# Performance work log

Measured on AMD Instinct MI355X. Metric: run time of the kernel, lower is better.

## Reference

```python
import jax, jax.numpy as jnp
import numpy as np

B, N, C = 16, 1024, 384
HEADS = 4
HIDDEN = 4 * C  # mlp_ratio=4 -> 1536
EPS = 1e-5


def layernorm(x, g, b):
    mu = jnp.mean(x, axis=-1, keepdims=True)
    var = jnp.mean((x - mu) ** 2, axis=-1, keepdims=True)
    return (x - mu) / jnp.sqrt(var + EPS) * g + b


def hardswish(x):
    return x * jnp.clip(x + 3.0, 0.0, 6.0) / 6.0


def setup_inputs() -> dict:
    key = jax.random.key(0)
    ks = jax.random.split(key, 8)
    s = 0.02
    return {
        "x": jax.random.normal(ks[0], (B, N, C), jnp.float32),
        "ln1_g": jnp.ones((C,), jnp.float32),
        "ln1_b": jnp.zeros((C,), jnp.float32),
        "Wqkv": jax.random.normal(ks[1], (3 * C, C), jnp.float32) * s,
        "Wproj": jax.random.normal(ks[2], (C, C), jnp.float32) * s,
        "bproj": jnp.zeros((C,), jnp.float32),
        "ln2_g": jnp.ones((C,), jnp.float32),
        "ln2_b": jnp.zeros((C,), jnp.float32),
        "Wfc1": jax.random.normal(ks[3], (HIDDEN, C, 1, 1), jnp.float32) * s,
        "bfc1": jnp.zeros((HIDDEN,), jnp.float32),
        "Wdw": jax.random.normal(ks[4], (HIDDEN, 1, 3, 3), jnp.float32) * s,
        "bdw": jnp.zeros((HIDDEN,), jnp.float32),
        "Wfc2": jax.random.normal(ks[5], (C, HIDDEN, 1, 1), jnp.float32) * s,
        "bfc2": jnp.zeros((C,), jnp.float32),
        "H": 32,
        "W": 32,
    }


def reference(x, ln1_g, ln1_b, Wqkv, Wproj, bproj, ln2_g, ln2_b,
              Wfc1, bfc1, Wdw, bdw, Wfc2, bfc2, H, W):
    b, n, c = x.shape
    h = HEADS
    hd = c // h
    # --- attention branch ---
    xn = layernorm(x, ln1_g, ln1_b)
    qkv = xn @ Wqkv.T  # [B,N,3C]
    qkv = qkv.reshape(b, n, h, 3, hd).transpose(3, 0, 2, 1, 4)  # [3,B,h,N,hd]
    q, k, v = qkv[0], qkv[1], qkv[2]
    attn = jax.nn.softmax(jnp.einsum('bhnd,bhmd->bhnm', q, k) * (hd ** -0.5), axis=-1)
    o = jnp.einsum('bhnm,bhmd->bhnd', attn, v)  # [B,h,N,hd]
    o = o.transpose(0, 2, 1, 3).reshape(b, n, c)
    o = o @ Wproj.T + bproj
    x = x + o
    # --- IRB (inverted residual conv MLP) branch ---
    y = layernorm(x, ln2_g, ln2_b)
    y = y.transpose(0, 2, 1).reshape(b, c, H, W)  # NCHW
    dn = ('NCHW', 'OIHW', 'NCHW')
    y = jax.lax.conv_general_dilated(y, Wfc1, (1, 1), 'VALID', dimension_numbers=dn)
    y = hardswish(y + bfc1[None, :, None, None])
    y = jax.lax.conv_general_dilated(y, Wdw, (1, 1), 'SAME',
                                     feature_group_count=Wdw.shape[0],
                                     dimension_numbers=dn)
    y = hardswish(y + bdw[None, :, None, None])
    y = jax.lax.conv_general_dilated(y, Wfc2, (1, 1), 'VALID', dimension_numbers=dn)
    y = y + bfc2[None, :, None, None]
    y = y.reshape(b, c, n).transpose(0, 2, 1)
    return x + y
```

## Files before the change

kernel.cpp:

```cpp
#include <hip/hip_runtime.h>
#include <hip/hip_bf16.h>
#include <math.h>

#define BB 16
#define NN 1024
#define CC 384
#define HEADS 4
#define HD 96
#define HID 1536
#define MROWS (BB*NN)

typedef __attribute__((ext_vector_type(8))) short bf16x8;
typedef __attribute__((ext_vector_type(4))) float f32x4;

__device__ __forceinline__ float hswish(float x) {
    float t = fminf(fmaxf(x + 3.0f, 0.0f), 6.0f);
    return x * t * (1.0f / 6.0f);
}

__device__ __forceinline__ ushort f2bf(float f) {
    union { float f; unsigned u; } v; v.f = f;
    unsigned r = v.u + 0x7fff + ((v.u >> 16) & 1);
    return (ushort)(r >> 16);
}

__device__ __forceinline__ float bf2f(ushort u) {
    union { unsigned u; float f; } v; v.u = ((unsigned)u) << 16;
    return v.f;
}

__device__ __forceinline__ void gload16(const ushort* g, ushort* l) {
    __builtin_amdgcn_global_load_lds(
        (const __attribute__((address_space(1))) void*)g,
        (__attribute__((address_space(3))) void*)l, 16, 0, 0);
}

#define S_QKV (1152*384)
#define S_P   (384*384)
#define S_1   (1536*384)
#define S_2   (384*1536)
__global__ __launch_bounds__(256) void wconv_all(
    const float* __restrict__ wqkv, const float* __restrict__ wproj,
    const float* __restrict__ wfc1, const float* __restrict__ wfc2,
    ushort* __restrict__ dq, ushort* __restrict__ dp,
    ushort* __restrict__ d1, ushort* __restrict__ d2)
{
    int i = blockIdx.x * 256 + threadIdx.x;
    if (i < S_QKV) {
        int row = i / 384;
        float v = wqkv[i];
        if ((row % 288) < 96) v *= 0.10206207261596577f;
        dq[i] = f2bf(v);
        return;
    }
    i -= S_QKV;
    if (i < S_P) { dp[i] = f2bf(wproj[i]); return; }
    i -= S_P;
    if (i < S_1) { d1[i] = f2bf(wfc1[i]); return; }
    i -= S_1;
    if (i < S_2) d2[i] = f2bf(wfc2[i]);
}

__global__ __launch_bounds__(256) void ln_kernel(
    const float* __restrict__ x, const float* __restrict__ g,
    const float* __restrict__ b, ushort* __restrict__ y)
{
    int row = blockIdx.x * 4 + (threadIdx.x >> 6);
    int lane = threadIdx.x & 63;
    const float* xr = x + (size_t)row * CC;
    float v[6];
    float s = 0.f;
#pragma unroll
    for (int j = 0; j < 6; ++j) { v[j] = xr[lane + 64 * j]; s += v[j]; }
#pragma unroll
    for (int off = 32; off; off >>= 1) s += __shfl_xor(s, off, 64);
    float mu = s * (1.0f / CC);
    float s2 = 0.f;
#pragma unroll
    for (int j = 0; j < 6; ++j) { float d = v[j] - mu; s2 += d * d; }
#pragma unroll
    for (int off = 32; off; off >>= 1) s2 += __shfl_xor(s2, off, 64);
    float rinv = rsqrtf(s2 * (1.0f / CC) + 1e-5f);
    ushort* yr = y + (size_t)row * CC;
#pragma unroll
    for (int j = 0; j < 6; ++j) {
        int c = lane + 64 * j;
        yr[c] = f2bf((v[j] - mu) * rinv * g[c] + b[c]);
    }
}

template<int BN>
__global__ __launch_bounds__(256) void gemm_mfma(
    const ushort* __restrict__ A, const ushort* __restrict__ B,
    const float* __restrict__ bias, const float* __restrict__ res,
    float* __restrict__ Cf, ushort* __restrict__ Cb,
    int M, int N, int K, int act)
{
    constexpr int NF = BN / 32;
    __shared__ ushort As[128][64];
    __shared__ ushort Bs[BN][64];
    int tid = threadIdx.x;
    int lane = tid & 63, w = tid >> 6;
    int wr = w >> 1, wc = w & 1;
    int g = lane >> 4, li = lane & 15;

    int nx = N / BN;
    int bid = blockIdx.x;
    int rr = bid & 7, qq = bid >> 3;
    int xx = qq % nx, yy = (qq / nx) * 8 + rr;
    int m0 = yy * 128, n0 = xx * BN;

    int srow = tid >> 3;
    int scol = ((tid & 7) ^ (srow & 7)) * 8;

    f32x4 acc[4][NF];
#pragma unroll
    for (int m = 0; m < 4; ++m)
#pragma unroll
        for (int n = 0; n < NF; ++n) acc[m][n] = (f32x4){0.f, 0.f, 0.f, 0.f};

    for (int k0 = 0; k0 < K; k0 += 64) {
        __syncthreads();
#pragma unroll
        for (int j = 0; j < 4; ++j)
            gload16(A + (size_t)(m0 + j * 32 + srow) * K + k0 + scol,
                    &As[j * 32 + w * 8][0]);
#pragma unroll
        for (int j = 0; j < BN / 32; ++j)
            gload16(B + (size_t)(n0 + j * 32 + srow) * K + k0 + scol,
                    &Bs[j * 32 + w * 8][0]);
        __syncthreads();
#pragma unroll
        for (int s = 0; s < 2; ++s) {
            bf16x8 af[4], bfr[NF];
#pragma unroll
            for (int m = 0; m < 4; ++m) {
                int row = wr * 64 + m * 16 + li;
                af[m] = *(const bf16x8*)&As[row][((s * 4 + g) ^ (row & 7)) * 8];
            }
#pragma unroll
            for (int n = 0; n < NF; ++n) {
                int row = wc * (BN / 2) + n * 16 + li;
                bfr[n] = *(const bf16x8*)&Bs[row][((s * 4 + g) ^ (row & 7)) * 8];
            }
            __builtin_amdgcn_s_setprio(1);
#pragma unroll
            for (int m = 0; m < 4; ++m)
#pragma unroll
                for (int n = 0; n < NF; ++n)
                    acc[m][n] = __builtin_amdgcn_mfma_f32_16x16x32_bf16(
                        af[m], bfr[n], acc[m][n], 0, 0, 0);
            __builtin_amdgcn_s_setprio(0);
        }
    }

#pragma unroll
    for (int m = 0; m < 4; ++m)
#pragma unroll
        for (int n = 0; n < NF; ++n) {
            int col = n0 + wc * (BN / 2) + n * 16 + li;
            float bv = bias ? bias[col] : 0.f;
#pragma unroll
            for (int r = 0; r < 4; ++r) {
                int row = m0 + wr * 64 + m * 16 + g * 4 + r;
                float v = acc[m][n][r] + bv;
                if (act == 1) v = hswish(v);
                if (res) v += res[(size_t)row * N + col];
                if (Cb) Cb[(size_t)row * N + col] = f2bf(v);
                else    Cf[(size_t)row * N + col] = v;
            }
        }
}

__global__ __launch_bounds__(256) void gemm_qkv(
    const ushort* __restrict__ A, const ushort* __restrict__ B,
    ushort* __restrict__ Qb, ushort* __restrict__ Kb, ushort* __restrict__ Vb,
    int M)
{
    constexpr int K = CC;
    __shared__ ushort As[128][64];
    __shared__ ushort Bs[128][64];
    int tid = threadIdx.x;
    int lane = tid & 63, w = tid >> 6;
    int wr = w >> 1, wc = w & 1;
    int g = lane >> 4, li = lane & 15;

    const int nx = 1152 / 128;
    int bid = blockIdx.x;
    int rr = bid & 7, qq = bid >> 3;
    int xx = qq % nx, yy = (qq / nx) * 8 + rr;
    int m0 = yy * 128, n0 = xx * 128;

    int srow = tid >> 3;
    int scol = ((tid & 7) ^ (srow & 7)) * 8;

    f32x4 acc[4][4];
#pragma unroll
    for (int m = 0; m < 4; ++m)
#pragma unroll
        for (int n = 0; n < 4; ++n) acc[m][n] = (f32x4){0.f, 0.f, 0.f, 0.f};

    for (int k0 = 0; k0 < K; k0 += 64) {
        __syncthreads();
#pragma unroll
        for (int j = 0; j < 4; ++j) {
            gload16(A + (size_t)(m0 + j * 32 + srow) * K + k0 + scol,
                    &As[j * 32 + w * 8][0]);
            gload16(B + (size_t)(n0 + j * 32 + srow) * K + k0 + scol,
                    &Bs[j * 32 + w * 8][0]);
        }
        __syncthreads();
#pragma unroll
        for (int s = 0; s < 2; ++s) {
            bf16x8 af[4], bfr[4];
#pragma unroll
            for (int m = 0; m < 4; ++m) {
                int row = wr * 64 + m * 16 + li;
                af[m] = *(const bf16x8*)&As[row][((s * 4 + g) ^ (row & 7)) * 8];
            }
#pragma unroll
            for (int n = 0; n < 4; ++n) {
                int row = wc * 64 + n * 16 + li;
                bfr[n] = *(const bf16x8*)&Bs[row][((s * 4 + g) ^ (row & 7)) * 8];
            }
            __builtin_amdgcn_s_setprio(1);
#pragma unroll
            for (int m = 0; m < 4; ++m)
#pragma unroll
                for (int n = 0; n < 4; ++n)
                    acc[m][n] = __builtin_amdgcn_mfma_f32_16x16x32_bf16(
                        af[m], bfr[n], acc[m][n], 0, 0, 0);
            __builtin_amdgcn_s_setprio(0);
        }
    }

#pragma unroll
    for (int m = 0; m < 4; ++m)
#pragma unroll
        for (int n = 0; n < 4; ++n) {
            int col = n0 + wc * 64 + n * 16 + li;
            int h = col / 288;
            int rem = col - h * 288;
            int which = rem / 96;
            int d = rem - which * 96;
            ushort* dst = which == 0 ? Qb : (which == 1 ? Kb : Vb);
#pragma unroll
            for (int r = 0; r < 4; ++r) {
                int row = m0 + wr * 64 + m * 16 + g * 4 + r;
                int b = row >> 10, ntok = row & 1023;
                int bh = b * HEADS + h;
                dst[((size_t)bh * NN + ntok) * HD + d] = f2bf(acc[m][n][r]);
            }
        }
}

__global__ __launch_bounds__(256) void conv_v(
    const ushort* __restrict__ Vb, ushort* __restrict__ Vt)
{
    __shared__ ushort vt[HD][136];
    int n0 = blockIdx.x * 128;
    int bh = blockIdx.y;
    const ushort* base = Vb + ((size_t)bh * NN + n0) * HD;
    for (int i = threadIdx.x; i < 128 * HD; i += 256) {
        int n = i / HD, d = i % HD;
        vt[d][n] = base[(size_t)n * HD + d];
    }
    __syncthreads();
    for (int i = threadIdx.x; i < HD * 128; i += 256) {
        int d = i / 128, n = i % 128;
        Vt[((size_t)bh * HD + d) * NN + n0 + n] = vt[d][n];
    }
}

#define KVT 64
#define KPAD 104
#define VPAD 72
#define PPAD 72

__global__ __launch_bounds__(256) void attn_mfma(
    const ushort* __restrict__ Qb, const ushort* __restrict__ Kb,
    const ushort* __restrict__ Vt, ushort* __restrict__ o)
{
    __shared__ ushort Klds[KVT][KPAD];
    __shared__ ushort Vlds[112][VPAD];
    __shared__ ushort Plds[4][16][PPAD];
    int tid = threadIdx.x;
    int lane = tid & 63, w = tid >> 6;
    int g = lane >> 4, li = lane & 15;
    int bid = blockIdx.x;
    int qt = bid >> 6, bh = bid & 63;
    int q0 = qt * 64;
    int b = bh >> 2, h = bh & 3;

    for (int i = tid; i < 16 * VPAD; i += 256) {
        int rr = i / VPAD, cc = i % VPAD;
        Vlds[96 + rr][cc] = (rr == 0 && cc < 64) ? (ushort)0x3F80 : (ushort)0;
    }

    const ushort* qrow = Qb + ((size_t)bh * NN + q0 + w * 16 + li) * HD;
    bf16x8 qf[3];
#pragma unroll
    for (int s = 0; s < 3; ++s)
        qf[s] = *(const bf16x8*)(qrow + s * 32 + g * 8);

    f32x4 oacc[7];
#pragma unroll
    for (int dt = 0; dt < 7; ++dt) oacc[dt] = (f32x4){0.f, 0.f, 0.f, 0.f};

    for (int t = 0; t < NN / KVT; ++t) {
        int n0 = t * KVT;
        __syncthreads();
        for (int i = tid; i < KVT * 12; i += 256) {
            int row = i / 12, ch = i % 12;
            *(bf16x8*)&Klds[row][ch * 8] =
                *(const bf16x8*)(Kb + ((size_t)bh * NN + n0 + row) * HD + ch * 8);
        }
        for (int i = tid; i < HD * 8; i += 256) {
            int d = i / 8, ch = i % 8;
            *(bf16x8*)&Vlds[d][ch * 8] =
                *(const bf16x8*)(Vt + ((size_t)bh * HD + d) * NN + n0 + ch * 8);
        }
        __syncthreads();

        f32x4 sacc[4];
#pragma unroll
        for (int c = 0; c < 4; ++c) sacc[c] = (f32x4){0.f, 0.f, 0.f, 0.f};
        __builtin_amdgcn_s_setprio(1);
#pragma unroll
        for (int s = 0; s < 3; ++s)
#pragma unroll
            for (int c = 0; c < 4; ++c) {
                bf16x8 kf = *(const bf16x8*)&Klds[c * 16 + li][s * 32 + g * 8];
                sacc[c] = __builtin_amdgcn_mfma_f32_16x16x32_bf16(qf[s], kf, sacc[c], 0, 0, 0);
            }
        __builtin_amdgcn_s_setprio(0);

#pragma unroll
        for (int r = 0; r < 4; ++r)
#pragma unroll
            for (int c = 0; c < 4; ++c)
                Plds[w][g * 4 + r][c * 16 + li] = f2bf(__expf(sacc[c][r]));

        __builtin_amdgcn_s_setprio(1);
#pragma unroll
        for (int sub = 0; sub < 2; ++sub) {
            bf16x8 pf = *(const bf16x8*)&Plds[w][li][sub * 32 + g * 8];
#pragma unroll
            for (int dt = 0; dt < 7; ++dt) {
                bf16x8 vf = *(const bf16x8*)&Vlds[dt * 16 + li][sub * 32 + g * 8];
                oacc[dt] = __builtin_amdgcn_mfma_f32_16x16x32_bf16(pf, vf, oacc[dt], 0, 0, 0);
            }
        }
        __builtin_amdgcn_s_setprio(0);
    }

    float inv[4];
#pragma unroll
    for (int r = 0; r < 4; ++r)
        inv[r] = 1.0f / __shfl(oacc[6][r], lane & 48, 64);
#pragma unroll
    for (int dt = 0; dt < 6; ++dt)
#pragma unroll
        for (int r = 0; r < 4; ++r) {
            int row = q0 + w * 16 + g * 4 + r;
            int col = h * HD + dt * 16 + li;
            o[(size_t)(b * NN + row) * CC + col] = f2bf(oacc[dt][r] * inv[r]);
        }
}

__global__ __launch_bounds__(256) void dw_kernel(
    const ushort* __restrict__ h1, const float* __restrict__ w,
    const float* __restrict__ bias, ushort* __restrict__ h2)
{
    int tid = threadIdx.x;
    int c0 = blockIdx.x * 256 + (tid & 63) * 4;
    int x = blockIdx.y * 4 + (tid >> 6);
    int b = blockIdx.z;
    const ushort* base = h1 + (size_t)b * NN * HID + c0;
    ushort* obase = h2 + (size_t)b * NN * HID + c0;

    float wv[4][9];
#pragma unroll
    for (int q = 0; q < 4; ++q)
#pragma unroll
        for (int k = 0; k < 9; ++k) wv[q][k] = w[(c0 + q) * 9 + k];
    float bv[4];
#pragma unroll
    for (int q = 0; q < 4; ++q) bv[q] = bias[c0 + q];

    bool xm = (x > 0), xp = (x < 31);

    float win[2][3][4];
#pragma unroll
    for (int a = 0; a < 2; ++a)
#pragma unroll
        for (int p = 0; p < 3; ++p)
#pragma unroll
            for (int q = 0; q < 4; ++q) win[a][p][q] = 0.f;

    {
        const ushort* rp = base + (size_t)x * HID;
        if (xm) { ushort4 u = *(const ushort4*)(rp - HID);
            win[1][0][0]=bf2f(u.x); win[1][0][1]=bf2f(u.y); win[1][0][2]=bf2f(u.z); win[1][0][3]=bf2f(u.w); }
        { ushort4 u = *(const ushort4*)rp;
            win[1][1][0]=bf2f(u.x); win[1][1][1]=bf2f(u.y); win[1][1][2]=bf2f(u.z); win[1][1][3]=bf2f(u.w); }
        if (xp) { ushort4 u = *(const ushort4*)(rp + HID);
            win[1][2][0]=bf2f(u.x); win[1][2][1]=bf2f(u.y); win[1][2][2]=bf2f(u.z); win[1][2][3]=bf2f(u.w); }
    }

#pragma unroll
    for (int y = 0; y < 32; ++y) {
        float nw[3][4];
#pragma unroll
        for (int p = 0; p < 3; ++p)
#pragma unroll
            for (int q = 0; q < 4; ++q) nw[p][q] = 0.f;
        if (y < 31) {
            const ushort* rp = base + (size_t)((y + 1) * 32 + x) * HID;
            if (xm) { ushort4 u = *(const ushort4*)(rp - HID);
                nw[0][0]=bf2f(u.x); nw[0][1]=bf2f(u.y); nw[0][2]=bf2f(u.z); nw[0][3]=bf2f(u.w); }
            { ushort4 u = *(const ushort4*)rp;
                nw[1][0]=bf2f(u.x); nw[1][1]=bf2f(u.y); nw[1][2]=bf2f(u.z); nw[1][3]=bf2f(u.w); }
            if (xp) { ushort4 u = *(const ushort4*)(rp + HID);
                nw[2][0]=bf2f(u.x); nw[2][1]=bf2f(u.y); nw[2][2]=bf2f(u.z); nw[2][3]=bf2f(u.w); }
        }
        ushort4 ov;
        ushort* po = (ushort*)&ov;
#pragma unroll
        for (int q = 0; q < 4; ++q) {
            float a = bv[q];
            a = fmaf(win[0][0][q], wv[q][0], a);
            a = fmaf(win[0][1][q], wv[q][1], a);
            a = fmaf(win[0][2][q], wv[q][2], a);
            a = fmaf(win[1][0][q], wv[q][3], a);
            a = fmaf(win[1][1][q], wv[q][4], a);
            a = fmaf(win[1][2][q], wv[q][5], a);
            a = fmaf(nw[0][q], wv[q][6], a);
            a = fmaf(nw[1][q], wv[q][7], a);
            a = fmaf(nw[2][q], wv[q][8], a);
            po[q] = f2bf(hswish(a));
        }
        *(ushort4*)&obase[(size_t)(y * 32 + x) * HID] = ov;
#pragma unroll
        for (int p = 0; p < 3; ++p)
#pragma unroll
            for (int q = 0; q < 4; ++q) {
                win[0][p][q] = win[1][p][q];
                win[1][p][q] = nw[p][q];
            }
    }
}

extern "C" void kernel_launch(void* const* d_in, const int* in_sizes, int n_in,
                              void* d_out, int out_size, void* d_ws, size_t ws_size,
                              hipStream_t stream) {
    const float* x     = (const float*)d_in[0];
    const float* ln1_g = (const float*)d_in[1];
    const float* ln1_b = (const float*)d_in[2];
    const float* Wqkv  = (const float*)d_in[3];
    const float* Wproj = (const float*)d_in[4];
    const float* bproj = (const float*)d_in[5];
    const float* ln2_g = (const float*)d_in[6];
    const float* ln2_b = (const float*)d_in[7];
    const float* Wfc1  = (const float*)d_in[8];
    const float* bfc1  = (const float*)d_in[9];
    const float* Wdw   = (const float*)d_in[10];
    const float* bdw   = (const float*)d_in[11];
    const float* Wfc2  = (const float*)d_in[12];
    const float* bfc2  = (const float*)d_in[13];
    float* out = (float*)d_out;

    const int M = MROWS;
    ushort* abuf = (ushort*)d_ws;
    ushort* Qb   = abuf + (size_t)M * 384;
    ushort* Kb   = Qb   + (size_t)M * 384;
    ushort* Vb   = Kb   + (size_t)M * 384;
    ushort* Vt   = Vb   + (size_t)M * 384;
    ushort* obuf = Vt   + (size_t)M * 384;
    ushort* h1   = obuf + (size_t)M * 384;
    ushort* h2   = h1   + (size_t)M * 1536;
    ushort* wq   = h2   + (size_t)M * 1536;
    ushort* wp   = wq   + 1152 * 384;
    ushort* w1   = wp   + 384 * 384;
    ushort* w2   = w1   + 1536 * 384;

    wconv_all<<<(S_QKV + S_P + S_1 + S_2 + 255) / 256, 256, 0, stream>>>(
        Wqkv, Wproj, Wfc1, Wfc2, wq, wp, w1, w2);

    ln_kernel<<<M / 4, 256, 0, stream>>>(x, ln1_g, ln1_b, abuf);
    gemm_qkv<<<(1152 / 128) * (M / 128), 256, 0, stream>>>(abuf, wq, Qb, Kb, Vb, M);
    conv_v<<<dim3(NN / 128, BB * HEADS), 256, 0, stream>>>(Vb, Vt);
    attn_mfma<<<1024, 256, 0, stream>>>(Qb, Kb, Vt, obuf);
    gemm_mfma<64><<<(CC / 64) * (M / 128), 256, 0, stream>>>(
        obuf, wp, bproj, x, out, nullptr, M, CC, CC, 0);
    ln_kernel<<<M / 4, 256, 0, stream>>>(out, ln2_g, ln2_b, abuf);
    gemm_mfma<128><<<(HID / 128) * (M / 128), 256, 0, stream>>>(
        abuf, w1, bfc1, nullptr, nullptr, h1, M, HID, CC, 1);
    dw_kernel<<<dim3(HID / 256, 8, BB), 256, 0, stream>>>(h1, Wdw, bdw, h2);
    gemm_mfma<64><<<(CC / 64) * (M / 128), 256, 0, stream>>>(
        h2, w2, bfc2, out, out, nullptr, M, CC, HID, 0);
}
```

Before: 241.7 us.

## Fuse V transpose into QKV GEMM epilogue, merge LN1 with weight prep, async attention loads

```diff
diff --git a/kernel.cpp b/kernel.cpp
--- a/kernel.cpp
+++ b/kernel.cpp
@@ -24,6 +24,11 @@
     return (ushort)(r >> 16);
 }
 
+__device__ __forceinline__ ushort f2bf_hw(float f) {
+    __hip_bfloat16 t = __float2bfloat16(f);
+    return *(ushort*)&t;
+}
+
 __device__ __forceinline__ float bf2f(ushort u) {
     union { unsigned u; float f; } v; v.u = ((unsigned)u) << 16;
     return v.f;
@@ -39,13 +44,50 @@
 #define S_P   (384*384)
 #define S_1   (1536*384)
 #define S_2   (384*1536)
-__global__ __launch_bounds__(256) void wconv_all(
+#define WBLKS ((S_QKV + S_P + S_1 + S_2 + 255) / 256)
+
+__device__ __forceinline__ void ln_body(
+    const float* __restrict__ x, const float* __restrict__ g,
+    const float* __restrict__ b, ushort* __restrict__ y, int row)
+{
+    int lane = threadIdx.x & 63;
+    const float* xr = x + (size_t)row * CC;
+    float v[6];
+    float s = 0.f;
+#pragma unroll
+    for (int j = 0; j < 6; ++j) { v[j] = xr[lane + 64 * j]; s += v[j]; }
+#pragma unroll
+    for (int off = 32; off; off >>= 1) s += __shfl_xor(s, off, 64);
+    float mu = s * (1.0f / CC);
+    float s2 = 0.f;
+#pragma unroll
+    for (int j = 0; j < 6; ++j) { float d = v[j] - mu; s2 += d * d; }
+#pragma unroll
+    for (int off = 32; off; off >>= 1) s2 += __shfl_xor(s2, off, 64);
+    float rinv = rsqrtf(s2 * (1.0f / CC) + 1e-5f);
+    ushort* yr = y + (size_t)row * CC;
+#pragma unroll
+    for (int j = 0; j < 6; ++j) {
+        int c = lane + 64 * j;
+        yr[c] = f2bf((v[j] - mu) * rinv * g[c] + b[c]);
+    }
+}
+
+__global__ __launch_bounds__(256) void prep(
     const float* __restrict__ wqkv, const float* __restrict__ wproj,
     const float* __restrict__ wfc1, const float* __restrict__ wfc2,
     ushort* __restrict__ dq, ushort* __restrict__ dp,
-    ushort* __restrict__ d1, ushort* __restrict__ d2)
-{
-    int i = blockIdx.x * 256 + threadIdx.x;
+    ushort* __restrict__ d1, ushort* __restrict__ d2,
+    const float* __restrict__ x, const float* __restrict__ g1,
+    const float* __restrict__ b1, ushort* __restrict__ y)
+{
+    int blk = blockIdx.x;
+    if (blk >= WBLKS) {
+        int row = (blk - WBLKS) * 4 + (threadIdx.x >> 6);
+        ln_body(x, g1, b1, y, row);
+        return;
+    }
+    int i = blk * 256 + threadIdx.x;
     if (i < S_QKV) {
         int row = i / 384;
         float v = wqkv[i];
@@ -66,27 +108,7 @@
     const float* __restrict__ b, ushort* __restrict__ y)
 {
     int row = blockIdx.x * 4 + (threadIdx.x >> 6);
-    int lane = threadIdx.x & 63;
-    const float* xr = x + (size_t)row * CC;
-    float v[6];
-    float s = 0.f;
-#pragma unroll
-    for (int j = 0; j < 6; ++j) { v[j] = xr[lane + 64 * j]; s += v[j]; }
-#pragma unroll
-    for (int off = 32; off; off >>= 1) s += __shfl_xor(s, off, 64);
-    float mu = s * (1.0f / CC);
-    float s2 = 0.f;
-#pragma unroll
-    for (int j = 0; j < 6; ++j) { float d = v[j] - mu; s2 += d * d; }
-#pragma unroll
-    for (int off = 32; off; off >>= 1) s2 += __shfl_xor(s2, off, 64);
-    float rinv = rsqrtf(s2 * (1.0f / CC) + 1e-5f);
-    ushort* yr = y + (size_t)row * CC;
-#pragma unroll
-    for (int j = 0; j < 6; ++j) {
-        int c = lane + 64 * j;
-        yr[c] = f2bf((v[j] - mu) * rinv * g[c] + b[c]);
-    }
+    ln_body(x, g, b, y, row);
 }
 
 template<int BN>
@@ -174,18 +196,20 @@
 
 __global__ __launch_bounds__(256) void gemm_qkv(
     const ushort* __restrict__ A, const ushort* __restrict__ B,
-    ushort* __restrict__ Qb, ushort* __restrict__ Kb, ushort* __restrict__ Vb,
+    ushort* __restrict__ Qb, ushort* __restrict__ Kb, ushort* __restrict__ Vt,
     int M)
 {
     constexpr int K = CC;
-    __shared__ ushort As[128][64];
-    __shared__ ushort Bs[128][64];
+    __shared__ ushort sh[128 * 64 * 2];
+    ushort* As = sh;
+    ushort* Bs = sh + 128 * 64;
+    ushort* VtS = sh;
     int tid = threadIdx.x;
     int lane = tid & 63, w = tid >> 6;
     int wr = w >> 1, wc = w & 1;
     int g = lane >> 4, li = lane & 15;
 
-    const int nx = 1152 / 128;
+    const int nx = 9;
     int bid = blockIdx.x;
     int rr = bid & 7, qq = bid >> 3;
     int xx = qq % nx, yy = (qq / nx) * 8 + rr;
@@ -205,9 +229,9 @@
 #pragma unroll
         for (int j = 0; j < 4; ++j) {
             gload16(A + (size_t)(m0 + j * 32 + srow) * K + k0 + scol,
-                    &As[j * 32 + w * 8][0]);
+                    &As[(j * 32 + w * 8) * 64]);
             gload16(B + (size_t)(n0 + j * 32 + srow) * K + k0 + scol,
-                    &Bs[j * 32 + w * 8][0]);
+                    &Bs[(j * 32 + w * 8) * 64]);
         }
         __syncthreads();
 #pragma unroll
@@ -216,12 +240,12 @@
 #pragma unroll
             for (int m = 0; m < 4; ++m) {
                 int row = wr * 64 + m * 16 + li;
-                af[m] = *(const bf16x8*)&As[row][((s * 4 + g) ^ (row & 7)) * 8];
+                af[m] = *(const bf16x8*)&As[row * 64 + ((s * 4 + g) ^ (row & 7)) * 8];
             }
 #pragma unroll
             for (int n = 0; n < 4; ++n) {
                 int row = wc * 64 + n * 16 + li;
-                bfr[n] = *(const bf16x8*)&Bs[row][((s * 4 + g) ^ (row & 7)) * 8];
+                bfr[n] = *(const bf16x8*)&Bs[row * 64 + ((s * 4 + g) ^ (row & 7)) * 8];
             }
             __builtin_amdgcn_s_setprio(1);
 #pragma unroll
@@ -233,6 +257,18 @@
             __builtin_amdgcn_s_setprio(0);
         }
     }
+
+    int d0 = 0, d1 = 0, hv = 0;
+#pragma unroll
+    for (int hh = 0; hh < 4; ++hh) {
+        int vlo = 192 + 288 * hh, vhi = 288 + 288 * hh;
+        int lo = n0 > vlo ? n0 : vlo;
+        int hi = (n0 + 128) < vhi ? (n0 + 128) : vhi;
+        if (hi > lo) { hv = hh; d0 = lo - vlo; d1 = hi - vlo; }
+    }
+    int b0 = m0 >> 10, ntok0 = m0 & 1023;
+
+    __syncthreads();
 
 #pragma unroll
     for (int m = 0; m < 4; ++m)
@@ -243,46 +279,44 @@
             int rem = col - h * 288;
             int which = rem / 96;
             int d = rem - which * 96;
-            ushort* dst = which == 0 ? Qb : (which == 1 ? Kb : Vb);
 #pragma unroll
             for (int r = 0; r < 4; ++r) {
-                int row = m0 + wr * 64 + m * 16 + g * 4 + r;
-                int b = row >> 10, ntok = row & 1023;
-                int bh = b * HEADS + h;
-                dst[((size_t)bh * NN + ntok) * HD + d] = f2bf(acc[m][n][r]);
-            }
-        }
-}
-
-__global__ __launch_bounds__(256) void conv_v(
-    const ushort* __restrict__ Vb, ushort* __restrict__ Vt)
-{
-    __shared__ ushort vt[HD][136];
-    int n0 = blockIdx.x * 128;
-    int bh = blockIdx.y;
-    const ushort* base = Vb + ((size_t)bh * NN + n0) * HD;
-    for (int i = threadIdx.x; i < 128 * HD; i += 256) {
-        int n = i / HD, d = i % HD;
-        vt[d][n] = base[(size_t)n * HD + d];
-    }
+                int row = wr * 64 + m * 16 + g * 4 + r;
+                ushort bv = f2bf(acc[m][n][r]);
+                if (which == 2) {
+                    VtS[row * 100 + (d - d0)] = bv;
+                } else {
+                    int tok = m0 + row;
+                    int bq = tok >> 10, ntok = tok & 1023;
+                    int bh = bq * HEADS + h;
+                    (which ? Kb : Qb)[((size_t)bh * NN + ntok) * HD + d] = bv;
+                }
+            }
+        }
     __syncthreads();
-    for (int i = threadIdx.x; i < HD * 128; i += 256) {
-        int d = i / 128, n = i % 128;
-        Vt[((size_t)bh * HD + d) * NN + n0 + n] = vt[d][n];
-    }
-}
-
-#define KVT 64
-#define KPAD 104
-#define VPAD 72
+
+    int dspan = d1 - d0;
+    int bhv = b0 * HEADS + hv;
+    for (int idx = tid; idx < dspan * 16; idx += 256) {
+        int dd = idx >> 4, u0 = (idx & 15) * 8;
+        bf16x8 val;
+#pragma unroll
+        for (int e = 0; e < 8; ++e)
+            val[e] = (short)VtS[(u0 + e) * 100 + dd];
+        *(bf16x8*)(Vt + ((size_t)bhv * HD + d0 + dd) * NN + ntok0 + u0) = val;
+    }
+}
+
+#define KSTR 128
+#define VSTR 64
 #define PPAD 72
 
 __global__ __launch_bounds__(256) void attn_mfma(
     const ushort* __restrict__ Qb, const ushort* __restrict__ Kb,
     const ushort* __restrict__ Vt, ushort* __restrict__ o)
 {
-    __shared__ ushort Klds[KVT][KPAD];
-    __shared__ ushort Vlds[112][VPAD];
+    __shared__ ushort Klds[64 * KSTR];
+    __shared__ ushort Vlds[112 * VSTR];
     __shared__ ushort Plds[4][16][PPAD];
     int tid = threadIdx.x;
     int lane = tid & 63, w = tid >> 6;
@@ -292,9 +326,9 @@
     int q0 = qt * 64;
     int b = bh >> 2, h = bh & 3;
 
-    for (int i = tid; i < 16 * VPAD; i += 256) {
-        int rr = i / VPAD, cc = i % VPAD;
-        Vlds[96 + rr][cc] = (rr == 0 && cc < 64) ? (ushort)0x3F80 : (ushort)0;
+    for (int i = tid; i < 16 * VSTR; i += 256) {
+        int rr = i / VSTR;
+        Vlds[(96 + rr) * VSTR + (i & 63)] = (rr == 0) ? (ushort)0x3F80 : (ushort)0;
     }
 
     const ushort* qrow = Qb + ((size_t)bh * NN + q0 + w * 16 + li) * HD;
@@ -307,18 +341,23 @@
 #pragma unroll
     for (int dt = 0; dt < 7; ++dt) oacc[dt] = (f32x4){0.f, 0.f, 0.f, 0.f};
 
-    for (int t = 0; t < NN / KVT; ++t) {
-        int n0 = t * KVT;
+    const size_t kbase = (size_t)bh * NN;
+    const size_t vbase = (size_t)bh * HD;
+
+    for (int t = 0; t < NN / 64; ++t) {
+        int n0 = t * 64;
         __syncthreads();
-        for (int i = tid; i < KVT * 12; i += 256) {
-            int row = i / 12, ch = i % 12;
-            *(bf16x8*)&Klds[row][ch * 8] =
-                *(const bf16x8*)(Kb + ((size_t)bh * NN + n0 + row) * HD + ch * 8);
-        }
-        for (int i = tid; i < HD * 8; i += 256) {
-            int d = i / 8, ch = i % 8;
-            *(bf16x8*)&Vlds[d][ch * 8] =
-                *(const bf16x8*)(Vt + ((size_t)bh * HD + d) * NN + n0 + ch * 8);
+#pragma unroll
+        for (int j = 0; j < 4; ++j) {
+            int row = w * 16 + j * 4 + (lane >> 4);
+            gload16(Kb + (kbase + n0 + row) * HD + (((lane & 15) ^ (row & 7)) << 3),
+                    &Klds[(w * 16 + j * 4) * KSTR]);
+        }
+#pragma unroll
+        for (int j = 0; j < 3; ++j) {
+            int row = w * 24 + j * 8 + (lane >> 3);
+            gload16(Vt + (vbase + row) * NN + n0 + (((lane & 7) ^ (row & 7)) << 3),
+                    &Vlds[(w * 24 + j * 8) * VSTR]);
         }
         __syncthreads();
 
@@ -330,7 +369,8 @@
         for (int s = 0; s < 3; ++s)
 #pragma unroll
             for (int c = 0; c < 4; ++c) {
-                bf16x8 kf = *(const bf16x8*)&Klds[c * 16 + li][s * 32 + g * 8];
+                bf16x8 kf = *(const bf16x8*)&Klds[(c * 16 + li) * KSTR +
+                                                  (((s * 4 + g) ^ (li & 7)) << 3)];
                 sacc[c] = __builtin_amdgcn_mfma_f32_16x16x32_bf16(qf[s], kf, sacc[c], 0, 0, 0);
             }
         __builtin_amdgcn_s_setprio(0);
@@ -339,7 +379,7 @@
         for (int r = 0; r < 4; ++r)
 #pragma unroll
             for (int c = 0; c < 4; ++c)
-                Plds[w][g * 4 + r][c * 16 + li] = f2bf(__expf(sacc[c][r]));
+                Plds[w][g * 4 + r][c * 16 + li] = f2bf_hw(__expf(sacc[c][r]));
 
         __builtin_amdgcn_s_setprio(1);
 #pragma unroll
@@ -347,7 +387,8 @@
             bf16x8 pf = *(const bf16x8*)&Plds[w][li][sub * 32 + g * 8];
 #pragma unroll
             for (int dt = 0; dt < 7; ++dt) {
-                bf16x8 vf = *(const bf16x8*)&Vlds[dt * 16 + li][sub * 32 + g * 8];
+                bf16x8 vf = *(const bf16x8*)&Vlds[(dt * 16 + li) * VSTR +
+                                                  (((sub * 4 + g) ^ (li & 7)) << 3)];
                 oacc[dt] = __builtin_amdgcn_mfma_f32_16x16x32_bf16(pf, vf, oacc[dt], 0, 0, 0);
             }
         }
@@ -364,7 +405,7 @@
         for (int r = 0; r < 4; ++r) {
             int row = q0 + w * 16 + g * 4 + r;
             int col = h * HD + dt * 16 + li;
-            o[(size_t)(b * NN + row) * CC + col] = f2bf(oacc[dt][r] * inv[r]);
+            o[(size_t)(b * NN + row) * CC + col] = f2bf_hw(oacc[dt][r] * inv[r]);
         }
 }
 
@@ -474,8 +515,7 @@
     ushort* abuf = (ushort*)d_ws;
     ushort* Qb   = abuf + (size_t)M * 384;
     ushort* Kb   = Qb   + (size_t)M * 384;
-    ushort* Vb   = Kb   + (size_t)M * 384;
-    ushort* Vt   = Vb   + (size_t)M * 384;
+    ushort* Vt   = Kb   + (size_t)M * 384;
     ushort* obuf = Vt   + (size_t)M * 384;
     ushort* h1   = obuf + (size_t)M * 384;
     ushort* h2   = h1   + (size_t)M * 1536;
@@ -484,12 +524,9 @@
     ushort* w1   = wp   + 384 * 384;
     ushort* w2   = w1   + 1536 * 384;
 
-    wconv_all<<<(S_QKV + S_P + S_1 + S_2 + 255) / 256, 256, 0, stream>>>(
-        Wqkv, Wproj, Wfc1, Wfc2, wq, wp, w1, w2);
-
-    ln_kernel<<<M / 4, 256, 0, stream>>>(x, ln1_g, ln1_b, abuf);
-    gemm_qkv<<<(1152 / 128) * (M / 128), 256, 0, stream>>>(abuf, wq, Qb, Kb, Vb, M);
-    conv_v<<<dim3(NN / 128, BB * HEADS), 256, 0, stream>>>(Vb, Vt);
+    prep<<<WBLKS + M / 4, 256, 0, stream>>>(
+        Wqkv, Wproj, Wfc1, Wfc2, wq, wp, w1, w2, x, ln1_g, ln1_b, abuf);
+    gemm_qkv<<<9 * (M / 128), 256, 0, stream>>>(abuf, wq, Qb, Kb, Vt, M);
     attn_mfma<<<1024, 256, 0, stream>>>(Qb, Kb, Vt, obuf);
     gemm_mfma<64><<<(CC / 64) * (M / 128), 256, 0, stream>>>(
         obuf, wp, bproj, x, out, nullptr, M, CC, CC, 0);
```

New measurement: 235.8 us. -2.5%, faster.
